# Kernel optimization log

Hardware: AMD Instinct MI355X
Metric: run time of the kernel (lower is better)

Reference implementation:

```python
import jax, jax.numpy as jnp
import numpy as np

N_NODES = 100000
N_EDGES = 1600000
IN_C, HID_C, OUT_C = 64, 64, 16


def _sage_conv(x, src, dst, W_l, b_l, W_r, num_nodes):
    # PyG SAGEConv (aggr='mean'): out = lin_l(mean_{j->i} x_j) + lin_r(x_i)
    # aggregate first (cheap small-d features), then one GEMM
    msg_sum = jax.ops.segment_sum(x[src], dst, num_segments=num_nodes)
    deg = jax.ops.segment_sum(jnp.ones_like(dst, dtype=x.dtype), dst,
                              num_segments=num_nodes)
    mean = msg_sum / jnp.maximum(deg, 1.0)[:, None]
    return mean @ W_l + b_l + x @ W_r


def setup_inputs() -> dict:
    key = jax.random.key(0)
    ks = jax.random.split(key, 8)
    x = jax.random.normal(ks[0], (N_NODES, IN_C), dtype=jnp.float32)
    edge_index = jax.random.randint(ks[1], (2, N_EDGES), 0, N_NODES, dtype=jnp.int64)
    # Glorot-ish init for weights; lin_l has bias, lin_r has none (PyG default)
    def glorot(k, fan_in, fan_out):
        s = jnp.sqrt(6.0 / (fan_in + fan_out))
        return jax.random.uniform(k, (fan_in, fan_out), jnp.float32, -s, s)
    return {
        "x": x,
        "edge_index": edge_index,
        "W1_l": glorot(ks[2], IN_C, HID_C),
        "b1": jnp.zeros((HID_C,), jnp.float32),
        "W1_r": glorot(ks[3], IN_C, HID_C),
        "W2_l": glorot(ks[4], HID_C, OUT_C),
        "b2": jnp.zeros((OUT_C,), jnp.float32),
        "W2_r": glorot(ks[5], HID_C, OUT_C),
    }


def reference(x, edge_index, W1_l, b1, W1_r, W2_l, b2, W2_r):
    src, dst = edge_index[0], edge_index[1]
    h = _sage_conv(x, src, dst, W1_l, b1, W1_r, N_NODES)
    h = jax.nn.relu(h)
    # dropout p=0.3 is identity in eval mode
    out = _sage_conv(h, src, dst, W2_l, b2, W2_r, N_NODES)
    return out
```

## Files before the change

kernel.cpp:

```cpp
#include <hip/hip_runtime.h>
#include <hip/hip_fp16.h>

#define N_NODES 100000
#define N_EDGES 1600000
#define IN_C 64
#define HID_C 64
#define OUT_C 16

#define BKT 256
#define BSH 8
#define NBKT 391
#define CAP 5120
#define GB 512
#define EPB 3125
#define G1B 1563

typedef _Float16 f16x8 __attribute__((ext_vector_type(8)));
typedef float f32x16 __attribute__((ext_vector_type(16)));

__global__ __launch_bounds__(256) void k_merged1(
    const int* __restrict__ src, const int* __restrict__ dst,
    int* __restrict__ gcnt, int* __restrict__ binned,
    const float* __restrict__ x, const float* __restrict__ Wl,
    const float* __restrict__ Wr, const float* __restrict__ b,
    __half* __restrict__ p, __half* __restrict__ q) {
  __shared__ _Float16 sA[64 * 68];
  __shared__ _Float16 sW[128 * 68];
  int t = threadIdx.x;

  if (blockIdx.x < GB) {
    int* h   = (int*)sA;
    int* cur = (int*)sW;
    for (int i = t; i < NBKT; i += 256) h[i] = 0;
    __syncthreads();
    int base = blockIdx.x * EPB;
    int end = base + EPB;
    for (int e = base + t; e < end; e += 256)
      atomicAdd(&h[dst[e] >> BSH], 1);
    __syncthreads();
    for (int i = t; i < NBKT; i += 256) {
      int c = h[i];
      int b0 = atomicAdd(&gcnt[i], c);
      cur[i] = i * CAP + b0;
    }
    __syncthreads();
    for (int e = base + t; e < end; e += 256) {
      int d = dst[e];
      int pos = atomicAdd(&cur[d >> BSH], 1);
      binned[pos] = (src[e] << BSH) | (d & (BKT - 1));
    }
    return;
  }

  int n0 = (blockIdx.x - GB) * 64;

  for (int f = t; f < 1024; f += 256) {
    int r = f >> 4, c4 = f & 15;
    int n = n0 + r;
    float4 v = {0.0f, 0.0f, 0.0f, 0.0f};
    if (n < N_NODES) v = *(const float4*)&x[(size_t)n * 64 + c4 * 4];
    union { _Float16 h[4]; float2 f2; } u;
    u.h[0] = (_Float16)v.x; u.h[1] = (_Float16)v.y;
    u.h[2] = (_Float16)v.z; u.h[3] = (_Float16)v.w;
    *(float2*)&sA[r * 68 + c4 * 4] = u.f2;
  }
  for (int f = t; f < 2048; f += 256) {
    int k = f >> 5, c4 = f & 31;
    float4 w = (c4 < 16) ? *(const float4*)&Wl[k * 64 + c4 * 4]
                         : *(const float4*)&Wr[k * 64 + (c4 - 16) * 4];
    int c = c4 * 4;
    sW[(c + 0) * 68 + k] = (_Float16)w.x;
    sW[(c + 1) * 68 + k] = (_Float16)w.y;
    sW[(c + 2) * 68 + k] = (_Float16)w.z;
    sW[(c + 3) * 68 + k] = (_Float16)w.w;
  }
  __syncthreads();

  int w = t >> 6, lane = t & 63;
  int m = lane & 31, half = lane >> 5;
  int rt = w & 1, cg = w >> 1;

  f32x16 acc[2];
#pragma unroll
  for (int r = 0; r < 16; ++r) { acc[0][r] = 0.0f; acc[1][r] = 0.0f; }

  const _Float16* pA = &sA[(rt * 32 + m) * 68 + half * 8];
  const _Float16* pB0 = &sW[(cg * 64 + m) * 68 + half * 8];
  const _Float16* pB1 = &sW[(cg * 64 + 32 + m) * 68 + half * 8];
#pragma unroll
  for (int kc = 0; kc < 4; ++kc) {
    union { f16x8 v; float2 f2[2]; } a, b0, b1;
    a.f2[0] = *(const float2*)(pA + kc * 16);
    a.f2[1] = *(const float2*)(pA + kc * 16 + 4);
    b0.f2[0] = *(const float2*)(pB0 + kc * 16);
    b0.f2[1] = *(const float2*)(pB0 + kc * 16 + 4);
    b1.f2[0] = *(const float2*)(pB1 + kc * 16);
    b1.f2[1] = *(const float2*)(pB1 + kc * 16 + 4);
    acc[0] = __builtin_amdgcn_mfma_f32_32x32x16_f16(a.v, b0.v, acc[0], 0, 0, 0);
    acc[1] = __builtin_amdgcn_mfma_f32_32x32x16_f16(a.v, b1.v, acc[1], 0, 0, 0);
  }

  if (cg == 0) {
#pragma unroll
    for (int tt = 0; tt < 2; ++tt) {
      int col = tt * 32 + m;
#pragma unroll
      for (int r = 0; r < 16; ++r) {
        int row = (r & 3) + 4 * half + 8 * (r >> 2);
        int n = n0 + rt * 32 + row;
        if (n < N_NODES) p[(size_t)n * 64 + col] = __float2half(acc[tt][r]);
      }
    }
  } else {
    float bias[2] = {b[m], b[32 + m]};
#pragma unroll
    for (int tt = 0; tt < 2; ++tt) {
      int col = tt * 32 + m;
#pragma unroll
      for (int r = 0; r < 16; ++r) {
        int row = (r & 3) + 4 * half + 8 * (r >> 2);
        int n = n0 + rt * 32 + row;
        if (n < N_NODES)
          q[(size_t)n * 64 + col] = __float2half(acc[tt][r] + bias[tt]);
      }
    }
  }
}

__global__ __launch_bounds__(512) void k_fuse1b(
    const float4* __restrict__ p1, const int* __restrict__ gcnt,
    const int* __restrict__ binned, int* __restrict__ csr,
    int* __restrict__ rowstart, int* __restrict__ cnt,
    float4* __restrict__ q1h) {
  __shared__ int hcnt[BKT];
  __shared__ int hscan[BKT];
  __shared__ int cur[BKT];
  __shared__ int lcsr[CAP];
  int b = blockIdx.x;
  int t = threadIdx.x;
  if (t < BKT) hcnt[t] = 0;
  __syncthreads();
  int start = b * CAP;
  int total = gcnt[b];
  for (int i = t; i < total; i += 512)
    atomicAdd(&hcnt[binned[start + i] & (BKT - 1)], 1);
  __syncthreads();
  int v = 0;
  if (t < BKT) {
    v = hcnt[t];
    hscan[t] = v;
  }
  __syncthreads();
  for (int st = 1; st < 256; st <<= 1) {
    int a = 0;
    if (t < BKT && t >= st) a = hscan[t - st];
    __syncthreads();
    if (t < BKT) hscan[t] += a;
    __syncthreads();
  }
  if (t < BKT) {
    cur[t] = hscan[t] - v;
    int n = (b << BSH) + t;
    if (n < N_NODES) {
      rowstart[n] = start + hscan[t] - v;
      cnt[n] = v;
    }
  }
  __syncthreads();
  for (int i = t; i < total; i += 512) {
    int vv = binned[start + i];
    int pos = atomicAdd(&cur[vv & (BKT - 1)], 1);
    lcsr[pos] = vv >> BSH;
  }
  __syncthreads();
  for (int i = t; i < total; i += 512) csr[start + i] = lcsr[i];

  int g = t >> 3, c4 = t & 7;
  for (int r = g; r < BKT; r += 64) {
    int n = (b << BSH) + r;
    if (n >= N_NODES) continue;
    int deg = hcnt[r];
    int row = hscan[r] - deg;
    float acc[8];
#pragma unroll
    for (int m = 0; m < 8; ++m) acc[m] = 0.0f;
    int j = 0;
    for (; j + 8 <= deg; j += 8) {
      int idx[8];
#pragma unroll
      for (int u = 0; u < 8; ++u) idx[u] = lcsr[row + j + u];
      float4 av[8];
#pragma unroll
      for (int u = 0; u < 8; ++u) av[u] = p1[idx[u] * 8 + c4];
#pragma unroll
      for (int u = 0; u < 8; ++u) {
        const __half2* h = (const __half2*)&av[u];
#pragma unroll
        for (int m = 0; m < 4; ++m) {
          float2 f = __half22float2(h[m]);
          acc[2 * m] += f.x;
          acc[2 * m + 1] += f.y;
        }
      }
    }
    for (; j < deg; ++j) {
      float4 a = p1[lcsr[row + j] * 8 + c4];
      const __half2* h = (const __half2*)&a;
#pragma unroll
      for (int m = 0; m < 4; ++m) {
        float2 f = __half22float2(h[m]);
        acc[2 * m] += f.x;
        acc[2 * m + 1] += f.y;
      }
    }
    float inv = 1.0f / fmaxf((float)deg, 1.0f);
    int o = n * 8 + c4;
    float4 qv = q1h[o];
    __half2* qh = (__half2*)&qv;
    float4 res;
    __half2* rh = (__half2*)&res;
#pragma unroll
    for (int m = 0; m < 4; ++m) {
      float2 f = __half22float2(qh[m]);
      float2 s;
      s.x = fmaxf(acc[2 * m] * inv + f.x, 0.0f);
      s.y = fmaxf(acc[2 * m + 1] * inv + f.y, 0.0f);
      rh[m] = __float22half2_rn(s);
    }
    q1h[o] = res;
  }
}

__global__ __launch_bounds__(256) void k_gemm2(
    const __half* __restrict__ h, const float* __restrict__ Wl,
    const float* __restrict__ Wr, const float* __restrict__ b,
    __half* __restrict__ p, float* __restrict__ q) {
  __shared__ _Float16 sA[128 * 68];
  __shared__ _Float16 sW[32 * 68];
  int t = threadIdx.x;
  int n0 = blockIdx.x * 128;

  for (int f = t; f < 2048; f += 256) {
    int r = f >> 4, c4 = f & 15;
    int n = n0 + r;
    float2 v = {0.0f, 0.0f};
    if (n < N_NODES) v = *(const float2*)&h[(size_t)n * 64 + c4 * 4];
    *(float2*)&sA[r * 68 + c4 * 4] = v;
  }
  for (int f = t; f < 512; f += 256) {
    int k = f >> 3, c4 = f & 7;
    float4 w = (c4 < 4) ? *(const float4*)&Wl[k * 16 + c4 * 4]
                        : *(const float4*)&Wr[k * 16 + (c4 - 4) * 4];
    int c = c4 * 4;
    sW[(c + 0) * 68 + k] = (_Float16)w.x;
    sW[(c + 1) * 68 + k] = (_Float16)w.y;
    sW[(c + 2) * 68 + k] = (_Float16)w.z;
    sW[(c + 3) * 68 + k] = (_Float16)w.w;
  }
  __syncthreads();

  int w = t >> 6, lane = t & 63;
  int m = lane & 31, half = lane >> 5;

  f32x16 acc;
#pragma unroll
  for (int r = 0; r < 16; ++r) acc[r] = 0.0f;

  const _Float16* pA = &sA[(w * 32 + m) * 68 + half * 8];
  const _Float16* pB = &sW[m * 68 + half * 8];
#pragma unroll
  for (int kc = 0; kc < 4; ++kc) {
    union { f16x8 v; float2 f2[2]; } a, bb;
    a.f2[0] = *(const float2*)(pA + kc * 16);
    a.f2[1] = *(const float2*)(pA + kc * 16 + 4);
    bb.f2[0] = *(const float2*)(pB + kc * 16);
    bb.f2[1] = *(const float2*)(pB + kc * 16 + 4);
    acc = __builtin_amdgcn_mfma_f32_32x32x16_f16(a.v, bb.v, acc, 0, 0, 0);
  }

  if (m < 16) {
#pragma unroll
    for (int r = 0; r < 16; ++r) {
      int row = (r & 3) + 4 * half + 8 * (r >> 2);
      int n = n0 + w * 32 + row;
      if (n < N_NODES) p[(size_t)n * 16 + m] = __float2half(acc[r]);
    }
  } else {
    float bias = b[m - 16];
#pragma unroll
    for (int r = 0; r < 16; ++r) {
      int row = (r & 3) + 4 * half + 8 * (r >> 2);
      int n = n0 + w * 32 + row;
      if (n < N_NODES) q[(size_t)n * 16 + (m - 16)] = acc[r] + bias;
    }
  }
}

__global__ __launch_bounds__(256) void k_fuse2(
    const float4* __restrict__ p2, const float4* __restrict__ q2,
    const int* __restrict__ rowstart, const int* __restrict__ cnt,
    const int* __restrict__ csr, float4* __restrict__ out) {
  int t = threadIdx.x;
  int n = blockIdx.x * 128 + (t >> 1);
  if (n >= N_NODES) return;
  int c8 = t & 1;
  int row = rowstart[n];
  int deg = cnt[n];
  float acc[8];
#pragma unroll
  for (int m = 0; m < 8; ++m) acc[m] = 0.0f;
  int j = 0;
  for (; j + 8 <= deg; j += 8) {
    int idx[8];
#pragma unroll
    for (int u = 0; u < 8; ++u) idx[u] = csr[row + j + u];
    float4 av[8];
#pragma unroll
    for (int u = 0; u < 8; ++u) av[u] = p2[idx[u] * 2 + c8];
#pragma unroll
    for (int u = 0; u < 8; ++u) {
      const __half2* h = (const __half2*)&av[u];
#pragma unroll
      for (int m = 0; m < 4; ++m) {
        float2 f = __half22float2(h[m]);
        acc[2 * m] += f.x;
        acc[2 * m + 1] += f.y;
      }
    }
  }
  for (; j < deg; ++j) {
    float4 a = p2[csr[row + j] * 2 + c8];
    const __half2* h = (const __half2*)&a;
#pragma unroll
    for (int m = 0; m < 4; ++m) {
      float2 f = __half22float2(h[m]);
      acc[2 * m] += f.x;
      acc[2 * m + 1] += f.y;
    }
  }
  float inv = 1.0f / fmaxf((float)deg, 1.0f);
  float4 q0 = q2[n * 4 + c8 * 2];
  float4 q1v = q2[n * 4 + c8 * 2 + 1];
  float4 o0 = {acc[0] * inv + q0.x, acc[1] * inv + q0.y,
               acc[2] * inv + q0.z, acc[3] * inv + q0.w};
  float4 o1 = {acc[4] * inv + q1v.x, acc[5] * inv + q1v.y,
               acc[6] * inv + q1v.z, acc[7] * inv + q1v.w};
  out[n * 4 + c8 * 2] = o0;
  out[n * 4 + c8 * 2 + 1] = o1;
}

extern "C" void kernel_launch(void* const* d_in, const int* in_sizes, int n_in,
                              void* d_out, int out_size, void* d_ws, size_t ws_size,
                              hipStream_t stream) {
  const float* x   = (const float*)d_in[0];
  const int* edge  = (const int*)d_in[1];
  const int* src   = edge;
  const int* dst   = edge + N_EDGES;
  const float* W1l = (const float*)d_in[2];
  const float* b1  = (const float*)d_in[3];
  const float* W1r = (const float*)d_in[4];
  const float* W2l = (const float*)d_in[5];
  const float* b2  = (const float*)d_in[6];
  const float* W2r = (const float*)d_in[7];
  float* out = (float*)d_out;

  int* gcnt     = (int*)d_ws;
  int* rowstart = gcnt + 512;
  int* cnt      = rowstart + N_NODES;
  int* binned   = cnt + N_NODES;
  int* csr      = binned + NBKT * CAP;
  __half* p1    = (__half*)(csr + NBKT * CAP);
  __half* q1h   = p1 + (size_t)N_NODES * 64;
  __half* p2    = p1;
  float* q2     = (float*)(p1 + (size_t)N_NODES * 16);

  hipMemsetAsync(gcnt, 0, NBKT * sizeof(int), stream);

  k_merged1<<<GB + G1B, 256, 0, stream>>>(src, dst, gcnt, binned,
                                          x, W1l, W1r, b1, p1, q1h);
  k_fuse1b<<<NBKT, 512, 0, stream>>>((const float4*)p1, gcnt, binned, csr,
                                     rowstart, cnt, (float4*)q1h);
  k_gemm2<<<(N_NODES + 127) / 128, 256, 0, stream>>>(q1h, W2l, W2r, b2, p2, q2);
  k_fuse2<<<(N_NODES + 127) / 128, 256, 0, stream>>>((const float4*)p2,
                                                     (const float4*)q2,
                                                     rowstart, cnt, csr,
                                                     (float4*)out);
}
```

Baseline: 193.0 us.

## Fuse layer-2 GEMM into layer-1 aggregation kernel via shared-memory tile

The separate layer-2 GEMM kernel is removed. Each bucket block of the aggregation kernel now writes its ReLU'd hidden rows into shared memory and immediately runs 16x16x32 MFMAs against W2_l/W2_r to produce p2 and q2. The block size doubles to 1024 threads so the 256-node tile is covered in fewer passes. This removes one launch and the global write and read of the hidden activations. In exchange, shared memory per block grows and occupancy drops, with only 391 blocks of 1024 threads available to hide the gather latency.

Result: faster. 189.0 us (-2.1%).

```diff
diff --git a/kernel.cpp b/kernel.cpp
--- a/kernel.cpp
+++ b/kernel.cpp
@@ -16,6 +16,7 @@
 #define G1B 1563
 
 typedef _Float16 f16x8 __attribute__((ext_vector_type(8)));
+typedef float f32x4 __attribute__((ext_vector_type(4)));
 typedef float f32x16 __attribute__((ext_vector_type(16)));
 
 __global__ __launch_bounds__(256) void k_merged1(
@@ -127,22 +128,38 @@
   }
 }
 
-__global__ __launch_bounds__(512) void k_fuse1b(
+__global__ __launch_bounds__(1024) void k_fuse1c(
     const float4* __restrict__ p1, const int* __restrict__ gcnt,
-    const int* __restrict__ binned, int* __restrict__ csr,
+    const int* __restrict__ binned, const float* __restrict__ W2l,
+    const float* __restrict__ W2r, const float* __restrict__ b2,
+    const float4* __restrict__ q1, int* __restrict__ csr,
     int* __restrict__ rowstart, int* __restrict__ cnt,
-    float4* __restrict__ q1h) {
+    __half* __restrict__ p2, float* __restrict__ q2) {
   __shared__ int hcnt[BKT];
   __shared__ int hscan[BKT];
   __shared__ int cur[BKT];
   __shared__ int lcsr[CAP];
+  __shared__ _Float16 sH[256 * 68];
+  __shared__ _Float16 sW[32 * 68];
   int b = blockIdx.x;
   int t = threadIdx.x;
+
+  if (t < 512) {
+    int k = t >> 3, c4v = t & 7;
+    float4 w = (c4v < 4) ? *(const float4*)&W2l[k * 16 + c4v * 4]
+                         : *(const float4*)&W2r[k * 16 + (c4v - 4) * 4];
+    int c = c4v * 4;
+    sW[(c + 0) * 68 + k] = (_Float16)w.x;
+    sW[(c + 1) * 68 + k] = (_Float16)w.y;
+    sW[(c + 2) * 68 + k] = (_Float16)w.z;
+    sW[(c + 3) * 68 + k] = (_Float16)w.w;
+  }
   if (t < BKT) hcnt[t] = 0;
   __syncthreads();
+
   int start = b * CAP;
   int total = gcnt[b];
-  for (int i = t; i < total; i += 512)
+  for (int i = t; i < total; i += 1024)
     atomicAdd(&hcnt[binned[start + i] & (BKT - 1)], 1);
   __syncthreads();
   int v = 0;
@@ -167,16 +184,16 @@
     }
   }
   __syncthreads();
-  for (int i = t; i < total; i += 512) {
+  for (int i = t; i < total; i += 1024) {
     int vv = binned[start + i];
     int pos = atomicAdd(&cur[vv & (BKT - 1)], 1);
     lcsr[pos] = vv >> BSH;
   }
   __syncthreads();
-  for (int i = t; i < total; i += 512) csr[start + i] = lcsr[i];
+  for (int i = t; i < total; i += 1024) csr[start + i] = lcsr[i];
 
   int g = t >> 3, c4 = t & 7;
-  for (int r = g; r < BKT; r += 64) {
+  for (int r = g; r < BKT; r += 128) {
     int n = (b << BSH) + r;
     if (n >= N_NODES) continue;
     int deg = hcnt[r];
@@ -214,84 +231,58 @@
       }
     }
     float inv = 1.0f / fmaxf((float)deg, 1.0f);
-    int o = n * 8 + c4;
-    float4 qv = q1h[o];
+    float4 qv = q1[n * 8 + c4];
     __half2* qh = (__half2*)&qv;
-    float4 res;
-    __half2* rh = (__half2*)&res;
-#pragma unroll
-    for (int m = 0; m < 4; ++m) {
+    union { __half2 h2[2]; float2 f2; } u01, u23;
+#pragma unroll
+    for (int m = 0; m < 2; ++m) {
       float2 f = __half22float2(qh[m]);
       float2 s;
       s.x = fmaxf(acc[2 * m] * inv + f.x, 0.0f);
       s.y = fmaxf(acc[2 * m + 1] * inv + f.y, 0.0f);
-      rh[m] = __float22half2_rn(s);
-    }
-    q1h[o] = res;
-  }
-}
-
-__global__ __launch_bounds__(256) void k_gemm2(
-    const __half* __restrict__ h, const float* __restrict__ Wl,
-    const float* __restrict__ Wr, const float* __restrict__ b,
-    __half* __restrict__ p, float* __restrict__ q) {
-  __shared__ _Float16 sA[128 * 68];
-  __shared__ _Float16 sW[32 * 68];
-  int t = threadIdx.x;
-  int n0 = blockIdx.x * 128;
-
-  for (int f = t; f < 2048; f += 256) {
-    int r = f >> 4, c4 = f & 15;
-    int n = n0 + r;
-    float2 v = {0.0f, 0.0f};
-    if (n < N_NODES) v = *(const float2*)&h[(size_t)n * 64 + c4 * 4];
-    *(float2*)&sA[r * 68 + c4 * 4] = v;
-  }
-  for (int f = t; f < 512; f += 256) {
-    int k = f >> 3, c4 = f & 7;
-    float4 w = (c4 < 4) ? *(const float4*)&Wl[k * 16 + c4 * 4]
-                        : *(const float4*)&Wr[k * 16 + (c4 - 4) * 4];
-    int c = c4 * 4;
-    sW[(c + 0) * 68 + k] = (_Float16)w.x;
-    sW[(c + 1) * 68 + k] = (_Float16)w.y;
-    sW[(c + 2) * 68 + k] = (_Float16)w.z;
-    sW[(c + 3) * 68 + k] = (_Float16)w.w;
-  }
-  __syncthreads();
-
-  int w = t >> 6, lane = t & 63;
-  int m = lane & 31, half = lane >> 5;
-
-  f32x16 acc;
-#pragma unroll
-  for (int r = 0; r < 16; ++r) acc[r] = 0.0f;
-
-  const _Float16* pA = &sA[(w * 32 + m) * 68 + half * 8];
-  const _Float16* pB = &sW[m * 68 + half * 8];
-#pragma unroll
-  for (int kc = 0; kc < 4; ++kc) {
-    union { f16x8 v; float2 f2[2]; } a, bb;
-    a.f2[0] = *(const float2*)(pA + kc * 16);
-    a.f2[1] = *(const float2*)(pA + kc * 16 + 4);
-    bb.f2[0] = *(const float2*)(pB + kc * 16);
-    bb.f2[1] = *(const float2*)(pB + kc * 16 + 4);
-    acc = __builtin_amdgcn_mfma_f32_32x32x16_f16(a.v, bb.v, acc, 0, 0, 0);
-  }
-
-  if (m < 16) {
-#pragma unroll
-    for (int r = 0; r < 16; ++r) {
-      int row = (r & 3) + 4 * half + 8 * (r >> 2);
-      int n = n0 + w * 32 + row;
-      if (n < N_NODES) p[(size_t)n * 16 + m] = __float2half(acc[r]);
-    }
-  } else {
-    float bias = b[m - 16];
-#pragma unroll
-    for (int r = 0; r < 16; ++r) {
-      int row = (r & 3) + 4 * half + 8 * (r >> 2);
-      int n = n0 + w * 32 + row;
-      if (n < N_NODES) q[(size_t)n * 16 + (m - 16)] = acc[r] + bias;
+      u01.h2[m] = __float22half2_rn(s);
+    }
+#pragma unroll
+    for (int m = 2; m < 4; ++m) {
+      float2 f = __half22float2(qh[m]);
+      float2 s;
+      s.x = fmaxf(acc[2 * m] * inv + f.x, 0.0f);
+      s.y = fmaxf(acc[2 * m + 1] * inv + f.y, 0.0f);
+      u23.h2[m - 2] = __float22half2_rn(s);
+    }
+    *(float2*)&sH[r * 68 + c4 * 8] = u01.f2;
+    *(float2*)&sH[r * 68 + c4 * 8 + 4] = u23.f2;
+  }
+  __syncthreads();
+
+  int wv = t >> 6, lane = t & 63;
+  int n16 = lane & 15, quad = lane >> 4;
+  f32x4 aP, aQ;
+#pragma unroll
+  for (int r = 0; r < 4; ++r) { aP[r] = 0.0f; aQ[r] = 0.0f; }
+  const _Float16* pA = &sH[(wv * 16 + n16) * 68 + quad * 8];
+  const _Float16* pBP = &sW[n16 * 68 + quad * 8];
+  const _Float16* pBQ = &sW[(16 + n16) * 68 + quad * 8];
+#pragma unroll
+  for (int kc = 0; kc < 2; ++kc) {
+    union { f16x8 v; float2 f2[2]; } a, bp, bq;
+    a.f2[0] = *(const float2*)(pA + kc * 32);
+    a.f2[1] = *(const float2*)(pA + kc * 32 + 4);
+    bp.f2[0] = *(const float2*)(pBP + kc * 32);
+    bp.f2[1] = *(const float2*)(pBP + kc * 32 + 4);
+    bq.f2[0] = *(const float2*)(pBQ + kc * 32);
+    bq.f2[1] = *(const float2*)(pBQ + kc * 32 + 4);
+    aP = __builtin_amdgcn_mfma_f32_16x16x32_f16(a.v, bp.v, aP, 0, 0, 0);
+    aQ = __builtin_amdgcn_mfma_f32_16x16x32_f16(a.v, bq.v, aQ, 0, 0, 0);
+  }
+  float bias = b2[n16];
+#pragma unroll
+  for (int r = 0; r < 4; ++r) {
+    int row = wv * 16 + quad * 4 + r;
+    int n = (b << BSH) + row;
+    if (n < N_NODES) {
+      p2[(size_t)n * 16 + n16] = __float2half(aP[r]);
+      q2[(size_t)n * 16 + n16] = aQ[r] + bias;
     }
   }
 }
@@ -370,17 +361,17 @@
   int* binned   = cnt + N_NODES;
   int* csr      = binned + NBKT * CAP;
   __half* p1    = (__half*)(csr + NBKT * CAP);
-  __half* q1h   = p1 + (size_t)N_NODES * 64;
-  __half* p2    = p1;
-  float* q2     = (float*)(p1 + (size_t)N_NODES * 16);
+  __half* q1    = p1 + (size_t)N_NODES * 64;
+  __half* p2    = q1 + (size_t)N_NODES * 64;
+  float* q2     = (float*)(p2 + (size_t)N_NODES * 16);
 
   hipMemsetAsync(gcnt, 0, NBKT * sizeof(int), stream);
 
   k_merged1<<<GB + G1B, 256, 0, stream>>>(src, dst, gcnt, binned,
-                                          x, W1l, W1r, b1, p1, q1h);
-  k_fuse1b<<<NBKT, 512, 0, stream>>>((const float4*)p1, gcnt, binned, csr,
-                                     rowstart, cnt, (float4*)q1h);
-  k_gemm2<<<(N_NODES + 127) / 128, 256, 0, stream>>>(q1h, W2l, W2r, b2, p2, q2);
+                                          x, W1l, W1r, b1, p1, q1);
+  k_fuse1c<<<NBKT, 1024, 0, stream>>>((const float4*)p1, gcnt, binned,
+                                      W2l, W2r, b2, (const float4*)q1,
+                                      csr, rowstart, cnt, p2, q2);
   k_fuse2<<<(N_NODES + 127) / 128, 256, 0, stream>>>((const float4*)p2,
                                                      (const float4*)q2,
                                                      rowstart, cnt, csr,
```
